# Performance work log

Measured on AMD Instinct MI355X. Metric: run time of the kernel, lower is better.

## Reference

```python
import jax, jax.numpy as jnp
import numpy as np

# config
HIDDEN = 1024
NUM_EXPERTS = 16
TOP_K = 4
MOE_INTER = 512
NUM_SHARED = 2
SHARED_INTER = MOE_INTER * NUM_SHARED  # 1024
NORM_TOPK = True
ROUTED_SCALE = 1.0
NUM_TOKENS = 1024


def setup_inputs() -> dict:
    key = jax.random.key(0)
    ks = jax.random.split(key, 8)
    s = 0.02
    return {
        "hidden_states": jax.random.normal(ks[0], (NUM_TOKENS, HIDDEN), jnp.float32),
        # router (BailingMoEGate): weight [E, H], no bias
        "router_w": jax.random.normal(ks[1], (NUM_EXPERTS, HIDDEN), jnp.float32) * s,
        # routed experts: gate/up proj [E, H, I], down proj [E, I, H]
        "w_gate": jax.random.normal(ks[2], (NUM_EXPERTS, HIDDEN, MOE_INTER), jnp.float32) * s,
        "w_up": jax.random.normal(ks[3], (NUM_EXPERTS, HIDDEN, MOE_INTER), jnp.float32) * s,
        "w_down": jax.random.normal(ks[4], (NUM_EXPERTS, MOE_INTER, HIDDEN), jnp.float32) * s,
        # shared experts (BailingMoEMLP, merged gate_up): [H, 2*Is], [Is, H]
        "ws_gate_up": jax.random.normal(ks[5], (HIDDEN, 2 * SHARED_INTER), jnp.float32) * s,
        "ws_down": jax.random.normal(ks[6], (SHARED_INTER, HIDDEN), jnp.float32) * s,
    }


def _moe_forward(x, router_w, w_gate, w_up, w_down, ws_gate_up, ws_down):
    T = x.shape[0]
    # ---- router: logits -> softmax -> top-k (score_function='softmax', no bias)
    logits = jnp.einsum("th,eh->te", x, router_w)          # [T, E]
    probs = jax.nn.softmax(logits, axis=-1)
    topk_w, topk_idx = jax.lax.top_k(probs, TOP_K)         # [T, K]
    if NORM_TOPK:
        topk_w = topk_w / jnp.sum(topk_w, axis=-1, keepdims=True)
    topk_w = topk_w * ROUTED_SCALE
    # sparse combine weights [T, E] (zeros for non-selected experts)
    combine = jnp.zeros((T, NUM_EXPERTS), x.dtype).at[
        jnp.arange(T)[:, None], topk_idx
    ].set(topk_w.astype(x.dtype))
    # ---- routed experts: SiLU(x W_gate) * (x W_up) then W_down, weighted combine
    g = jnp.einsum("th,ehi->tei", x, w_gate)               # [T, E, I]
    u = jnp.einsum("th,ehi->tei", x, w_up)
    h = jax.nn.silu(g) * u
    routed = jnp.einsum("tei,eih,te->th", h, w_down, combine)
    # ---- shared experts (dense SwiGLU MLP)
    gu = x @ ws_gate_up                                    # [T, 2*Is]
    g_s, u_s = jnp.split(gu, 2, axis=-1)
    shared = (jax.nn.silu(g_s) * u_s) @ ws_down
    return routed + shared


def reference(hidden_states, router_w, w_gate, w_up, w_down, ws_gate_up, ws_down):
    return _moe_forward(hidden_states, router_w, w_gate, w_up, w_down,
                        ws_gate_up, ws_down)
```

## Files before the change

kernel.cpp:

```cpp
#include <hip/hip_runtime.h>
#include <stdint.h>


typedef __attribute__((ext_vector_type(8))) unsigned short ushort8;
typedef __attribute__((ext_vector_type(4))) float f32x4;
typedef __attribute__((ext_vector_type(8))) __bf16 bf16x8;

#define T_TOK 1024
#define HID   1024
#define NEXP  16
#define TOPK  4
#define MINTER 512
#define SINTER 1024

constexpr size_t OFF_COUNTS = 0;
constexpr size_t OFF_LIST   = 1024;
constexpr size_t OFF_WT     = OFF_LIST  + 65536;
constexpr size_t OFF_TIDX   = OFF_WT    + 65536;
constexpr size_t OFF_XB     = OFF_TIDX  + 65536;
constexpr size_t OFF_HS     = OFF_XB    + 2097152;
constexpr size_t OFF_HR     = OFF_HS    + 2097152;
constexpr size_t OFF_WGT    = OFF_HR    + 4194304;
constexpr size_t OFF_WUT    = OFF_WGT   + 16777216;
constexpr size_t OFF_WDT    = OFF_WUT   + 16777216;
constexpr size_t OFF_WSGUT  = OFF_WDT   + 16777216;
constexpr size_t OFF_WSDT   = OFF_WSGUT + 4194304;
constexpr size_t OFF_ROUT   = OFF_WGT;

__device__ __forceinline__ unsigned short f2bf(float f) {
  union { float f; uint32_t u; } v; v.f = f;
  uint32_t r = (v.u + 0x7FFFu + ((v.u >> 16) & 1u)) >> 16;
  return (unsigned short)r;
}
__device__ __forceinline__ float bfu2f(uint32_t u) {
  union { uint32_t u; float f; } v; v.u = u << 16; return v.f;
}
__device__ __forceinline__ bf16x8 as_bf16x8(ushort8 s) {
  union { ushort8 s; bf16x8 b; } u; u.s = s; return u.b;
}
__device__ __forceinline__ float silu(float g) { return g / (1.f + __expf(-g)); }

__device__ __forceinline__ void glds16(const unsigned short* g, unsigned short* l) {
  __builtin_amdgcn_global_load_lds(
      (const __attribute__((address_space(1))) unsigned int*)g,
      (__attribute__((address_space(3))) unsigned int*)l, 16, 0, 0);
}

__global__ void init_kernel(int* counts) {
  if (threadIdx.x < NEXP) counts[threadIdx.x] = 0;
}

__global__ __launch_bounds__(64) void router_kernel(
    const float* __restrict__ x, const float* __restrict__ rw,
    int* counts, int* list, float* wt, int* tIdx,
    unsigned short* __restrict__ Xb) {
  const int t = blockIdx.x, l = threadIdx.x;
  float xv[16];
#pragma unroll
  for (int j = 0; j < 16; j++) xv[j] = x[t * HID + j * 64 + l];
#pragma unroll
  for (int j = 0; j < 16; j++) Xb[t * HID + j * 64 + l] = f2bf(xv[j]);
  float p[NEXP];
#pragma unroll
  for (int e = 0; e < NEXP; e++) {
    float s = 0.f;
#pragma unroll
    for (int j = 0; j < 16; j++) s += xv[j] * rw[e * HID + j * 64 + l];
#pragma unroll
    for (int off = 32; off > 0; off >>= 1) s += __shfl_xor(s, off);
    p[e] = s;
  }
  float mx = p[0];
#pragma unroll
  for (int e = 1; e < NEXP; e++) mx = fmaxf(mx, p[e]);
  int idx[TOPK]; float w4[TOPK]; float wsum = 0.f; unsigned used = 0u;
#pragma unroll
  for (int k = 0; k < TOPK; k++) {
    float bv = -1e30f; int bi = 0;
#pragma unroll
    for (int e = 0; e < NEXP; e++)
      if (!((used >> e) & 1u) && p[e] > bv) { bv = p[e]; bi = e; }
    used |= 1u << bi;
    idx[k] = bi;
    w4[k] = __expf(p[bi] - mx);
    wsum += w4[k];
  }
  const float inv = 1.f / wsum;
  if (l < TOPK) {
    const int e = idx[l];
    const int pos = atomicAdd(&counts[e], 1);
    list[e * 1024 + pos] = t;
    wt[e * 1024 + pos]   = w4[l] * inv;
    tIdx[t * TOPK + l]   = (e << 10) | pos;
  }
}

__global__ __launch_bounds__(256) void transpose_all_kernel(
    const float* __restrict__ Wg, const float* __restrict__ Wu,
    const float* __restrict__ Wd, const float* __restrict__ Wsgu,
    const float* __restrict__ Wsd,
    unsigned short* __restrict__ WgT, unsigned short* __restrict__ WuT,
    unsigned short* __restrict__ WdT, unsigned short* __restrict__ WsguT,
    unsigned short* __restrict__ WsdT) {
  const int bid = blockIdx.x;
  const float* src; unsigned short* dst; int R, C, tx, ty; size_t bo;
  if (bid < 4096) {
    const int which = bid >> 11, loc = bid & 2047;
    const int b = loc >> 7, t8 = loc & 127;
    src = which ? Wu : Wg; dst = which ? WuT : WgT;
    R = 1024; C = 512; bo = (size_t)b * R * C;
    tx = t8 & 7; ty = t8 >> 3;
  } else if (bid < 6144) {
    const int loc = bid - 4096, b = loc >> 7, t8 = loc & 127;
    src = Wd; dst = WdT; R = 512; C = 1024; bo = (size_t)b * R * C;
    tx = t8 & 15; ty = t8 >> 4;
  } else if (bid < 6656) {
    const int loc = bid - 6144;
    src = Wsgu; dst = WsguT; R = 1024; C = 2048; bo = 0;
    tx = loc & 31; ty = loc >> 5;
  } else {
    const int loc = bid - 6656;
    src = Wsd; dst = WsdT; R = 1024; C = 1024; bo = 0;
    tx = loc & 15; ty = loc >> 4;
  }
  __shared__ float tile[64][65];
  const int c0 = tx * 64, r0 = ty * 64, t = threadIdx.x;
  {
    const int r = t >> 4, c4 = (t & 15) * 4;
#pragma unroll
    for (int p = 0; p < 4; p++) {
      const int rr = p * 16 + r;
      const float4 v = *(const float4*)(src + bo + (size_t)(r0 + rr) * C + c0 + c4);
      tile[rr][c4 + 0] = v.x; tile[rr][c4 + 1] = v.y;
      tile[rr][c4 + 2] = v.z; tile[rr][c4 + 3] = v.w;
    }
  }
  __syncthreads();
  {
    const int c = t >> 2, rb = (t & 3) * 16;
#pragma unroll
    for (int s = 0; s < 4; s++) {
      const int rr = rb + 4 * s;
      union { unsigned short u[4]; uint2 v; } pk;
#pragma unroll
      for (int i = 0; i < 4; i++) pk.u[i] = f2bf(tile[rr + i][c]);
      *(uint2*)(dst + bo + (size_t)(c0 + c) * R + r0 + rr) = pk.v;
    }
  }
}

__global__ __launch_bounds__(256, 2) void phase1_kernel(
    const unsigned short* __restrict__ Xb,
    const unsigned short* __restrict__ WgT,
    const unsigned short* __restrict__ WuT,
    const unsigned short* __restrict__ WsguT,
    const int* __restrict__ counts, const int* __restrict__ list,
    const float* __restrict__ wt,
    unsigned short* __restrict__ Hr,
    unsigned short* __restrict__ Hs) {
  const int z = blockIdx.z, x = blockIdx.x, y = blockIdx.y;
  const bool routed = (z < NEXP);
  int cnt = 0, base = 0;
  if (routed) {
    if (x >= 4) return;
    cnt = counts[z];
    if (y * 128 >= cnt) return;
#pragma unroll
    for (int i = 0; i < NEXP; i++) base += (i < z) ? counts[i] : 0;
  }
  __shared__ __align__(16) unsigned short sA[2][128 * 32];
  __shared__ __align__(16) unsigned short sB[2][256 * 32];
  const int tid = threadIdx.x, w = tid >> 6, l = tid & 63;
  const int wm = w >> 1, wn = w & 1, m0 = y * 128;
  const int lg = ((l & 3) ^ ((l >> 3) & 3)) * 8;

  const unsigned short* aP[2];
#pragma unroll
  for (int ii = 0; ii < 2; ii++) {
    const int r = (2 * w + ii) * 16 + (l >> 2);
    const unsigned short* row;
    if (routed) row = Xb + (size_t)list[z * 1024 + min(m0 + r, cnt - 1)] * HID;
    else        row = Xb + (size_t)(m0 + r) * HID;
    aP[ii] = row + lg;
  }
  const unsigned short* bP[4];
#pragma unroll
  for (int ii = 0; ii < 4; ii++) {
    const int R = (4 * w + ii) * 16 + (l >> 2);
    const int col = x * 128 + (R & 127);
    const unsigned short* row;
    if (routed)
      row = ((R >= 128) ? WuT : WgT) + ((size_t)z * MINTER + col) * HID;
    else
      row = WsguT + ((size_t)((R >= 128) ? SINTER : 0) + col) * HID;
    bP[ii] = row + lg;
  }

  int aoff[4], boff[4];
#pragma unroll
  for (int i = 0; i < 4; i++) {
    const int m = wm * 64 + 16 * i + (l & 15);
    aoff[i] = m * 32 + (((l >> 4) ^ ((m >> 1) & 3)) * 8);
  }
#pragma unroll
  for (int j = 0; j < 4; j++) {
    const int n = wn * 64 + 16 * j + (l & 15);
    boff[j] = n * 32 + (((l >> 4) ^ ((n >> 1) & 3)) * 8);
  }

  f32x4 accG[4][4], accU[4][4];
#pragma unroll
  for (int i = 0; i < 4; i++)
#pragma unroll
    for (int j = 0; j < 4; j++) {
      accG[i][j] = (f32x4){0.f, 0.f, 0.f, 0.f};
      accU[i][j] = (f32x4){0.f, 0.f, 0.f, 0.f};
    }

  auto stage = [&](int k0, int bi) {
    unsigned short* A = sA[bi]; unsigned short* B = sB[bi];
#pragma unroll
    for (int ii = 0; ii < 2; ii++) glds16(aP[ii] + k0, A + (2 * w + ii) * 512);
#pragma unroll
    for (int ii = 0; ii < 4; ii++) glds16(bP[ii] + k0, B + (4 * w + ii) * 512);
  };

  stage(0, 0);
  const int steps = HID / 32;
  for (int s = 0; s < steps; s++) {
    __syncthreads();
    if (s + 1 < steps) stage((s + 1) * 32, (s + 1) & 1);
    const unsigned short* A = sA[s & 1];
    const unsigned short* B = sB[s & 1];
    bf16x8 af[4];
#pragma unroll
    for (int i = 0; i < 4; i++) af[i] = as_bf16x8(*(const ushort8*)(A + aoff[i]));
#pragma unroll
    for (int j = 0; j < 4; j++) {
      const bf16x8 gf = as_bf16x8(*(const ushort8*)(B + boff[j]));
      const bf16x8 uf = as_bf16x8(*(const ushort8*)(B + 128 * 32 + boff[j]));
#pragma unroll
      for (int i = 0; i < 4; i++) {
        accG[i][j] = __builtin_amdgcn_mfma_f32_16x16x32_bf16(af[i], gf, accG[i][j], 0, 0, 0);
        accU[i][j] = __builtin_amdgcn_mfma_f32_16x16x32_bf16(af[i], uf, accU[i][j], 0, 0, 0);
      }
    }
  }

#pragma unroll
  for (int i = 0; i < 4; i++)
#pragma unroll
    for (int r = 0; r < 4; r++) {
      const int row = wm * 64 + 16 * i + (l >> 4) * 4 + r;
      const int grow = m0 + row;
      if (routed) {
        if (grow < cnt) {
          const float wrow = wt[z * 1024 + grow];
#pragma unroll
          for (int j = 0; j < 4; j++) {
            const int col = x * 128 + wn * 64 + 16 * j + (l & 15);
            const float h = silu(accG[i][j][r]) * accU[i][j][r] * wrow;
            Hr[(size_t)(base + grow) * MINTER + col] = f2bf(h);
          }
        }
      } else {
#pragma unroll
        for (int j = 0; j < 4; j++) {
          const int col = x * 128 + wn * 64 + 16 * j + (l & 15);
          const float h = silu(accG[i][j][r]) * accU[i][j][r];
          Hs[(size_t)grow * SINTER + col] = f2bf(h);
        }
      }
    }
}

__global__ __launch_bounds__(256, 2) void phase2_kernel(
    const unsigned short* __restrict__ Hr, const unsigned short* __restrict__ Hs,
    const unsigned short* __restrict__ WdT,
    const unsigned short* __restrict__ WsdT,
    const int* __restrict__ counts,
    unsigned short* __restrict__ Rout,
    float* __restrict__ out) {
  const int z = blockIdx.z, x = blockIdx.x, y = blockIdx.y;
  const bool routed = (z < NEXP);
  int cnt = 0, base = 0, kdim;
  if (routed) {
    cnt = counts[z];
    if (y * 128 >= cnt) return;
#pragma unroll
    for (int i = 0; i < NEXP; i++) base += (i < z) ? counts[i] : 0;
    kdim = MINTER;
  } else {
    kdim = SINTER;
  }
  __shared__ __align__(16) unsigned short sA[2][128 * 32];
  __shared__ __align__(16) unsigned short sB[2][256 * 32];
  const int tid = threadIdx.x, w = tid >> 6, l = tid & 63;
  const int wm = w >> 1, wn = w & 1, m0 = y * 128;
  const int lg = ((l & 3) ^ ((l >> 3) & 3)) * 8;

  const unsigned short* aP[2];
#pragma unroll
  for (int ii = 0; ii < 2; ii++) {
    const int r = (2 * w + ii) * 16 + (l >> 2);
    const unsigned short* row;
    if (routed) row = Hr + (size_t)(base + min(m0 + r, cnt - 1)) * MINTER;
    else        row = Hs + (size_t)(m0 + r) * SINTER;
    aP[ii] = row + lg;
  }
  const unsigned short* bP[4];
#pragma unroll
  for (int ii = 0; ii < 4; ii++) {
    const int R = (4 * w + ii) * 16 + (l >> 2);
    const int col = x * 256 + R;
    const unsigned short* row =
        routed ? (WdT + ((size_t)z * HID + col) * MINTER)
               : (WsdT + (size_t)col * SINTER);
    bP[ii] = row + lg;
  }

  int aoff[4], boff[8];
#pragma unroll
  for (int i = 0; i < 4; i++) {
    const int m = wm * 64 + 16 * i + (l & 15);
    aoff[i] = m * 32 + (((l >> 4) ^ ((m >> 1) & 3)) * 8);
  }
#pragma unroll
  for (int j = 0; j < 8; j++) {
    const int n = wn * 128 + 16 * j + (l & 15);
    boff[j] = n * 32 + (((l >> 4) ^ ((n >> 1) & 3)) * 8);
  }

  f32x4 acc[4][8];
#pragma unroll
  for (int i = 0; i < 4; i++)
#pragma unroll
    for (int j = 0; j < 8; j++) acc[i][j] = (f32x4){0.f, 0.f, 0.f, 0.f};

  auto stage = [&](int k0, int bi) {
    unsigned short* A = sA[bi]; unsigned short* B = sB[bi];
#pragma unroll
    for (int ii = 0; ii < 2; ii++) glds16(aP[ii] + k0, A + (2 * w + ii) * 512);
#pragma unroll
    for (int ii = 0; ii < 4; ii++) glds16(bP[ii] + k0, B + (4 * w + ii) * 512);
  };

  stage(0, 0);
  const int steps = kdim / 32;
  for (int s = 0; s < steps; s++) {
    __syncthreads();
    if (s + 1 < steps) stage((s + 1) * 32, (s + 1) & 1);
    const unsigned short* A = sA[s & 1];
    const unsigned short* B = sB[s & 1];
    bf16x8 af[4];
#pragma unroll
    for (int i = 0; i < 4; i++) af[i] = as_bf16x8(*(const ushort8*)(A + aoff[i]));
#pragma unroll
    for (int j = 0; j < 8; j++) {
      const bf16x8 bfv = as_bf16x8(*(const ushort8*)(B + boff[j]));
#pragma unroll
      for (int i = 0; i < 4; i++)
        acc[i][j] = __builtin_amdgcn_mfma_f32_16x16x32_bf16(af[i], bfv, acc[i][j], 0, 0, 0);
    }
  }

#pragma unroll
  for (int i = 0; i < 4; i++)
#pragma unroll
    for (int r = 0; r < 4; r++) {
      const int row = wm * 64 + 16 * i + (l >> 4) * 4 + r;
      const int grow = m0 + row;
      if (routed) {
        if (grow < cnt) {
#pragma unroll
          for (int j = 0; j < 8; j++) {
            const int col = x * 256 + wn * 128 + 16 * j + (l & 15);
            Rout[(size_t)(base + grow) * HID + col] = f2bf(acc[i][j][r]);
          }
        }
      } else {
#pragma unroll
        for (int j = 0; j < 8; j++) {
          const int col = x * 256 + wn * 128 + 16 * j + (l & 15);
          out[(size_t)grow * HID + col] = acc[i][j][r];
        }
      }
    }
}

__global__ __launch_bounds__(256) void combine_kernel(
    const unsigned short* __restrict__ Rout, const int* __restrict__ counts,
    const int* __restrict__ tIdx, float* __restrict__ out) {
  __shared__ int sb[NEXP];
  if (threadIdx.x == 0) {
    int s = 0;
#pragma unroll
    for (int e = 0; e < NEXP; e++) { sb[e] = s; s += counts[e]; }
  }
  __syncthreads();
  const int t = blockIdx.x, c4 = threadIdx.x * 4;
  float4 o = *(const float4*)(out + (size_t)t * HID + c4);
#pragma unroll
  for (int k = 0; k < TOPK; k++) {
    const int v = tIdx[t * TOPK + k];
    const int row = sb[v >> 10] + (v & 1023);
    const uint2 rv = *(const uint2*)(Rout + (size_t)row * HID + c4);
    o.x += bfu2f(rv.x & 0xffffu); o.y += bfu2f(rv.x >> 16);
    o.z += bfu2f(rv.y & 0xffffu); o.w += bfu2f(rv.y >> 16);
  }
  *(float4*)(out + (size_t)t * HID + c4) = o;
}

extern "C" void kernel_launch(void* const* d_in, const int* in_sizes, int n_in,
                              void* d_out, int out_size, void* d_ws, size_t ws_size,
                              hipStream_t stream) {
  const float* x      = (const float*)d_in[0];
  const float* rw     = (const float*)d_in[1];
  const float* w_gate = (const float*)d_in[2];
  const float* w_up   = (const float*)d_in[3];
  const float* w_down = (const float*)d_in[4];
  const float* ws_gu  = (const float*)d_in[5];
  const float* ws_dn  = (const float*)d_in[6];
  float* out = (float*)d_out;
  char* ws = (char*)d_ws;

  int*   counts = (int*)  (ws + OFF_COUNTS);
  int*   list   = (int*)  (ws + OFF_LIST);
  float* wtbuf  = (float*)(ws + OFF_WT);
  int*   tIdx   = (int*)  (ws + OFF_TIDX);
  unsigned short* Xb    = (unsigned short*)(ws + OFF_XB);
  unsigned short* Hs    = (unsigned short*)(ws + OFF_HS);
  unsigned short* Hr    = (unsigned short*)(ws + OFF_HR);
  unsigned short* WgT   = (unsigned short*)(ws + OFF_WGT);
  unsigned short* WuT   = (unsigned short*)(ws + OFF_WUT);
  unsigned short* WdT   = (unsigned short*)(ws + OFF_WDT);
  unsigned short* WsguT = (unsigned short*)(ws + OFF_WSGUT);
  unsigned short* WsdT  = (unsigned short*)(ws + OFF_WSDT);
  unsigned short* Rout  = (unsigned short*)(ws + OFF_ROUT);

  init_kernel<<<1, 64, 0, stream>>>(counts);
  router_kernel<<<T_TOK, 64, 0, stream>>>(x, rw, counts, list, wtbuf, tIdx, Xb);
  transpose_all_kernel<<<6912, 256, 0, stream>>>(
      w_gate, w_up, w_down, ws_gu, ws_dn, WgT, WuT, WdT, WsguT, WsdT);
  phase1_kernel<<<dim3(8, 8, 17), 256, 0, stream>>>(
      Xb, WgT, WuT, WsguT, counts, list, wtbuf, Hr, Hs);
  phase2_kernel<<<dim3(4, 8, 17), 256, 0, stream>>>(
      Hr, Hs, WdT, WsdT, counts, Rout, out);
  combine_kernel<<<T_TOK, 256, 0, stream>>>(Rout, counts, tIdx, out);
  (void)in_sizes; (void)n_in; (void)out_size; (void)ws_size;
}
```

Measured before the change: 296.3 us.

## Replace LDS-staged GEMM tiles with direct global-to-register triple-buffered loads

Both expert GEMM kernels stop staging A and B tiles through shared memory with global_load_lds and barriers. Each wave now loads its MFMA fragments straight from global memory into registers, keeping a three-deep register pipeline, and launch bounds drop to one block per SIMD slot to free registers. This removes LDS traffic and __syncthreads, but tiles are no longer shared across waves, so each wave re-reads data from global memory or cache. The loads are strided 16-byte per lane rather than coalesced, and occupancy is lower.

```diff
diff --git a/kernel.cpp b/kernel.cpp
--- a/kernel.cpp
+++ b/kernel.cpp
@@ -39,12 +39,6 @@
   union { ushort8 s; bf16x8 b; } u; u.s = s; return u.b;
 }
 __device__ __forceinline__ float silu(float g) { return g / (1.f + __expf(-g)); }
-
-__device__ __forceinline__ void glds16(const unsigned short* g, unsigned short* l) {
-  __builtin_amdgcn_global_load_lds(
-      (const __attribute__((address_space(1))) unsigned int*)g,
-      (__attribute__((address_space(3))) unsigned int*)l, 16, 0, 0);
-}
 
 __global__ void init_kernel(int* counts) {
   if (threadIdx.x < NEXP) counts[threadIdx.x] = 0;
@@ -149,7 +143,7 @@
   }
 }
 
-__global__ __launch_bounds__(256, 2) void phase1_kernel(
+__global__ __launch_bounds__(256, 1) void phase1_kernel(
     const unsigned short* __restrict__ Xb,
     const unsigned short* __restrict__ WgT,
     const unsigned short* __restrict__ WuT,
@@ -168,44 +162,28 @@
 #pragma unroll
     for (int i = 0; i < NEXP; i++) base += (i < z) ? counts[i] : 0;
   }
-  __shared__ __align__(16) unsigned short sA[2][128 * 32];
-  __shared__ __align__(16) unsigned short sB[2][256 * 32];
   const int tid = threadIdx.x, w = tid >> 6, l = tid & 63;
   const int wm = w >> 1, wn = w & 1, m0 = y * 128;
-  const int lg = ((l & 3) ^ ((l >> 3) & 3)) * 8;
-
-  const unsigned short* aP[2];
-#pragma unroll
-  for (int ii = 0; ii < 2; ii++) {
-    const int r = (2 * w + ii) * 16 + (l >> 2);
-    const unsigned short* row;
-    if (routed) row = Xb + (size_t)list[z * 1024 + min(m0 + r, cnt - 1)] * HID;
-    else        row = Xb + (size_t)(m0 + r) * HID;
-    aP[ii] = row + lg;
-  }
-  const unsigned short* bP[4];
-#pragma unroll
-  for (int ii = 0; ii < 4; ii++) {
-    const int R = (4 * w + ii) * 16 + (l >> 2);
-    const int col = x * 128 + (R & 127);
-    const unsigned short* row;
-    if (routed)
-      row = ((R >= 128) ? WuT : WgT) + ((size_t)z * MINTER + col) * HID;
-    else
-      row = WsguT + ((size_t)((R >= 128) ? SINTER : 0) + col) * HID;
-    bP[ii] = row + lg;
-  }
-
-  int aoff[4], boff[4];
+  const int kq = (l >> 4) * 8;
+
+  const unsigned short* aP[4];
 #pragma unroll
   for (int i = 0; i < 4; i++) {
-    const int m = wm * 64 + 16 * i + (l & 15);
-    aoff[i] = m * 32 + (((l >> 4) ^ ((m >> 1) & 3)) * 8);
-  }
+    const int row = m0 + wm * 64 + 16 * i + (l & 15);
+    if (routed) aP[i] = Xb + (size_t)list[z * 1024 + min(row, cnt - 1)] * HID + kq;
+    else        aP[i] = Xb + (size_t)row * HID + kq;
+  }
+  const unsigned short *gP[4], *uP[4];
 #pragma unroll
   for (int j = 0; j < 4; j++) {
-    const int n = wn * 64 + 16 * j + (l & 15);
-    boff[j] = n * 32 + (((l >> 4) ^ ((n >> 1) & 3)) * 8);
+    const int n = x * 128 + wn * 64 + 16 * j + (l & 15);
+    if (routed) {
+      gP[j] = WgT + ((size_t)z * MINTER + n) * HID + kq;
+      uP[j] = WuT + ((size_t)z * MINTER + n) * HID + kq;
+    } else {
+      gP[j] = WsguT + (size_t)n * HID + kq;
+      uP[j] = WsguT + (size_t)(SINTER + n) * HID + kq;
+    }
   }
 
   f32x4 accG[4][4], accU[4][4];
@@ -217,35 +195,35 @@
       accU[i][j] = (f32x4){0.f, 0.f, 0.f, 0.f};
     }
 
-  auto stage = [&](int k0, int bi) {
-    unsigned short* A = sA[bi]; unsigned short* B = sB[bi];
-#pragma unroll
-    for (int ii = 0; ii < 2; ii++) glds16(aP[ii] + k0, A + (2 * w + ii) * 512);
-#pragma unroll
-    for (int ii = 0; ii < 4; ii++) glds16(bP[ii] + k0, B + (4 * w + ii) * 512);
-  };
-
-  stage(0, 0);
+  ushort8 Af[3][4], Gf[3][4], Uf[3][4];
+#define P1_LD(st, k0)                                                   \
+  {                                                                     \
+    _Pragma("unroll") for (int i = 0; i < 4; i++)                       \
+        Af[st][i] = *(const ushort8*)(aP[i] + (k0));                    \
+    _Pragma("unroll") for (int j = 0; j < 4; j++) {                     \
+      Gf[st][j] = *(const ushort8*)(gP[j] + (k0));                      \
+      Uf[st][j] = *(const ushort8*)(uP[j] + (k0));                      \
+    }                                                                   \
+  }
+  P1_LD(0, 0) P1_LD(1, 32) P1_LD(2, 64)
   const int steps = HID / 32;
+#pragma unroll 1
   for (int s = 0; s < steps; s++) {
-    __syncthreads();
-    if (s + 1 < steps) stage((s + 1) * 32, (s + 1) & 1);
-    const unsigned short* A = sA[s & 1];
-    const unsigned short* B = sB[s & 1];
-    bf16x8 af[4];
-#pragma unroll
-    for (int i = 0; i < 4; i++) af[i] = as_bf16x8(*(const ushort8*)(A + aoff[i]));
+    const int cur = s % 3;
 #pragma unroll
     for (int j = 0; j < 4; j++) {
-      const bf16x8 gf = as_bf16x8(*(const ushort8*)(B + boff[j]));
-      const bf16x8 uf = as_bf16x8(*(const ushort8*)(B + 128 * 32 + boff[j]));
+      const bf16x8 gf = as_bf16x8(Gf[cur][j]);
+      const bf16x8 uf = as_bf16x8(Uf[cur][j]);
 #pragma unroll
       for (int i = 0; i < 4; i++) {
-        accG[i][j] = __builtin_amdgcn_mfma_f32_16x16x32_bf16(af[i], gf, accG[i][j], 0, 0, 0);
-        accU[i][j] = __builtin_amdgcn_mfma_f32_16x16x32_bf16(af[i], uf, accU[i][j], 0, 0, 0);
+        const bf16x8 af = as_bf16x8(Af[cur][i]);
+        accG[i][j] = __builtin_amdgcn_mfma_f32_16x16x32_bf16(af, gf, accG[i][j], 0, 0, 0);
+        accU[i][j] = __builtin_amdgcn_mfma_f32_16x16x32_bf16(af, uf, accU[i][j], 0, 0, 0);
       }
     }
-  }
+    if (s + 3 < steps) P1_LD(cur, (s + 3) * 32)
+  }
+#undef P1_LD
 
 #pragma unroll
   for (int i = 0; i < 4; i++)
@@ -274,7 +252,7 @@
     }
 }
 
-__global__ __launch_bounds__(256, 2) void phase2_kernel(
+__global__ __launch_bounds__(256, 1) void phase2_kernel(
     const unsigned short* __restrict__ Hr, const unsigned short* __restrict__ Hs,
     const unsigned short* __restrict__ WdT,
     const unsigned short* __restrict__ WsdT,
@@ -293,42 +271,23 @@
   } else {
     kdim = SINTER;
   }
-  __shared__ __align__(16) unsigned short sA[2][128 * 32];
-  __shared__ __align__(16) unsigned short sB[2][256 * 32];
   const int tid = threadIdx.x, w = tid >> 6, l = tid & 63;
   const int wm = w >> 1, wn = w & 1, m0 = y * 128;
-  const int lg = ((l & 3) ^ ((l >> 3) & 3)) * 8;
-
-  const unsigned short* aP[2];
-#pragma unroll
-  for (int ii = 0; ii < 2; ii++) {
-    const int r = (2 * w + ii) * 16 + (l >> 2);
-    const unsigned short* row;
-    if (routed) row = Hr + (size_t)(base + min(m0 + r, cnt - 1)) * MINTER;
-    else        row = Hs + (size_t)(m0 + r) * SINTER;
-    aP[ii] = row + lg;
-  }
-  const unsigned short* bP[4];
-#pragma unroll
-  for (int ii = 0; ii < 4; ii++) {
-    const int R = (4 * w + ii) * 16 + (l >> 2);
-    const int col = x * 256 + R;
-    const unsigned short* row =
-        routed ? (WdT + ((size_t)z * HID + col) * MINTER)
-               : (WsdT + (size_t)col * SINTER);
-    bP[ii] = row + lg;
-  }
-
-  int aoff[4], boff[8];
+  const int kq = (l >> 4) * 8;
+
+  const unsigned short* aP[4];
 #pragma unroll
   for (int i = 0; i < 4; i++) {
-    const int m = wm * 64 + 16 * i + (l & 15);
-    aoff[i] = m * 32 + (((l >> 4) ^ ((m >> 1) & 3)) * 8);
-  }
+    const int row = m0 + wm * 64 + 16 * i + (l & 15);
+    if (routed) aP[i] = Hr + (size_t)(base + min(row, cnt - 1)) * MINTER + kq;
+    else        aP[i] = Hs + (size_t)row * SINTER + kq;
+  }
+  const unsigned short* bP[8];
 #pragma unroll
   for (int j = 0; j < 8; j++) {
-    const int n = wn * 128 + 16 * j + (l & 15);
-    boff[j] = n * 32 + (((l >> 4) ^ ((n >> 1) & 3)) * 8);
+    const int n = x * 256 + wn * 128 + 16 * j + (l & 15);
+    bP[j] = routed ? (WdT + ((size_t)z * HID + n) * MINTER + kq)
+                   : (WsdT + (size_t)n * SINTER + kq);
   }
 
   f32x4 acc[4][8];
@@ -337,32 +296,31 @@
 #pragma unroll
     for (int j = 0; j < 8; j++) acc[i][j] = (f32x4){0.f, 0.f, 0.f, 0.f};
 
-  auto stage = [&](int k0, int bi) {
-    unsigned short* A = sA[bi]; unsigned short* B = sB[bi];
-#pragma unroll
-    for (int ii = 0; ii < 2; ii++) glds16(aP[ii] + k0, A + (2 * w + ii) * 512);
-#pragma unroll
-    for (int ii = 0; ii < 4; ii++) glds16(bP[ii] + k0, B + (4 * w + ii) * 512);
-  };
-
-  stage(0, 0);
+  ushort8 Af[3][4], Bf[3][8];
+#define P2_LD(st, k0)                                                   \
+  {                                                                     \
+    _Pragma("unroll") for (int i = 0; i < 4; i++)                       \
+        Af[st][i] = *(const ushort8*)(aP[i] + (k0));                    \
+    _Pragma("unroll") for (int j = 0; j < 8; j++)                       \
+        Bf[st][j] = *(const ushort8*)(bP[j] + (k0));                    \
+  }
+  P2_LD(0, 0) P2_LD(1, 32) P2_LD(2, 64)
   const int steps = kdim / 32;
+#pragma unroll 1
   for (int s = 0; s < steps; s++) {
-    __syncthreads();
-    if (s + 1 < steps) stage((s + 1) * 32, (s + 1) & 1);
-    const unsigned short* A = sA[s & 1];
-    const unsigned short* B = sB[s & 1];
-    bf16x8 af[4];
-#pragma unroll
-    for (int i = 0; i < 4; i++) af[i] = as_bf16x8(*(const ushort8*)(A + aoff[i]));
+    const int cur = s % 3;
 #pragma unroll
     for (int j = 0; j < 8; j++) {
-      const bf16x8 bfv = as_bf16x8(*(const ushort8*)(B + boff[j]));
-#pragma unroll
-      for (int i = 0; i < 4; i++)
-        acc[i][j] = __builtin_amdgcn_mfma_f32_16x16x32_bf16(af[i], bfv, acc[i][j], 0, 0, 0);
-    }
-  }
+      const bf16x8 bfv = as_bf16x8(Bf[cur][j]);
+#pragma unroll
+      for (int i = 0; i < 4; i++) {
+        const bf16x8 af = as_bf16x8(Af[cur][i]);
+        acc[i][j] = __builtin_amdgcn_mfma_f32_16x16x32_bf16(af, bfv, acc[i][j], 0, 0, 0);
+      }
+    }
+    if (s + 3 < steps) P2_LD(cur, (s + 3) * 32)
+  }
+#undef P2_LD
 
 #pragma unroll
   for (int i = 0; i < 4; i++)
```

After: 770.0 us. 2.6x slower.

## Triple-buffer GEMM LDS pipeline with explicit vmcnt waits and drop swizzle

Applied to the files above, without the earlier changes.

Both grouped GEMM kernels move from a double-buffered LDS pipeline with __syncthreads to a three-stage ring. Loads are issued two steps ahead and gated with an explicit s_waitcnt vmcnt(12) plus barrier, so more global-to-LDS traffic stays in flight. The XOR swizzle on LDS offsets is removed, which can raise bank conflicts, and the weight-transpose kernel now writes 16-byte packed stores instead of 8-byte ones. The larger LDS footprint (about 72KB per block) may limit the two-blocks-per-CU occupancy target, and the wrapped prefetch at the tail issues redundant loads.

```diff
diff --git a/kernel.cpp b/kernel.cpp
--- a/kernel.cpp
+++ b/kernel.cpp
@@ -45,6 +45,9 @@
       (const __attribute__((address_space(1))) unsigned int*)g,
       (__attribute__((address_space(3))) unsigned int*)l, 16, 0, 0);
 }
+
+#define PIPE_WAIT() asm volatile("s_waitcnt vmcnt(12)\ns_barrier" ::: "memory")
+#define PIPE_SYNC() asm volatile("s_waitcnt lgkmcnt(0)\ns_barrier" ::: "memory")
 
 __global__ void init_kernel(int* counts) {
   if (threadIdx.x < NEXP) counts[threadIdx.x] = 0;
@@ -136,16 +139,13 @@
     }
   }
   __syncthreads();
-  {
-    const int c = t >> 2, rb = (t & 3) * 16;
-#pragma unroll
-    for (int s = 0; s < 4; s++) {
-      const int rr = rb + 4 * s;
-      union { unsigned short u[4]; uint2 v; } pk;
-#pragma unroll
-      for (int i = 0; i < 4; i++) pk.u[i] = f2bf(tile[rr + i][c]);
-      *(uint2*)(dst + bo + (size_t)(c0 + c) * R + r0 + rr) = pk.v;
-    }
+#pragma unroll
+  for (int half = 0; half < 2; half++) {
+    const int c = half * 32 + (t >> 3), r8 = (t & 7) * 8;
+    union { unsigned short u[8]; ushort8 v; } pk;
+#pragma unroll
+    for (int i = 0; i < 8; i++) pk.u[i] = f2bf(tile[r8 + i][c]);
+    *(ushort8*)(dst + bo + (size_t)(c0 + c) * R + r0 + r8) = pk.v;
   }
 }
 
@@ -168,45 +168,36 @@
 #pragma unroll
     for (int i = 0; i < NEXP; i++) base += (i < z) ? counts[i] : 0;
   }
-  __shared__ __align__(16) unsigned short sA[2][128 * 32];
-  __shared__ __align__(16) unsigned short sB[2][256 * 32];
+  __shared__ __align__(16) unsigned short sA[3][128 * 32];
+  __shared__ __align__(16) unsigned short sB[3][256 * 32];
   const int tid = threadIdx.x, w = tid >> 6, l = tid & 63;
   const int wm = w >> 1, wn = w & 1, m0 = y * 128;
-  const int lg = ((l & 3) ^ ((l >> 3) & 3)) * 8;
-
-  const unsigned short* aP[2];
+
+  const unsigned short* aS[2];
 #pragma unroll
   for (int ii = 0; ii < 2; ii++) {
-    const int r = (2 * w + ii) * 16 + (l >> 2);
+    const int r = 32 * w + 16 * ii + (l >> 2);
     const unsigned short* row;
     if (routed) row = Xb + (size_t)list[z * 1024 + min(m0 + r, cnt - 1)] * HID;
     else        row = Xb + (size_t)(m0 + r) * HID;
-    aP[ii] = row + lg;
-  }
-  const unsigned short* bP[4];
+    aS[ii] = row + (l & 3) * 8;
+  }
+  const unsigned short* bS[4];
 #pragma unroll
   for (int ii = 0; ii < 4; ii++) {
-    const int R = (4 * w + ii) * 16 + (l >> 2);
+    const int R = 64 * w + 16 * ii + (l >> 2);
     const int col = x * 128 + (R & 127);
     const unsigned short* row;
-    if (routed)
-      row = ((R >= 128) ? WuT : WgT) + ((size_t)z * MINTER + col) * HID;
-    else
-      row = WsguT + ((size_t)((R >= 128) ? SINTER : 0) + col) * HID;
-    bP[ii] = row + lg;
-  }
-
-  int aoff[4], boff[4];
-#pragma unroll
-  for (int i = 0; i < 4; i++) {
-    const int m = wm * 64 + 16 * i + (l & 15);
-    aoff[i] = m * 32 + (((l >> 4) ^ ((m >> 1) & 3)) * 8);
-  }
-#pragma unroll
-  for (int j = 0; j < 4; j++) {
-    const int n = wn * 64 + 16 * j + (l & 15);
-    boff[j] = n * 32 + (((l >> 4) ^ ((n >> 1) & 3)) * 8);
-  }
+    if (routed) row = ((R >= 128) ? WuT : WgT) + ((size_t)z * MINTER + col) * HID;
+    else        row = WsguT + (size_t)(((R >= 128) ? SINTER : 0) + col) * HID;
+    bS[ii] = row + (l & 3) * 8;
+  }
+
+  int aOff[4], bOff[4];
+#pragma unroll
+  for (int i = 0; i < 4; i++) aOff[i] = (wm * 64 + 16 * i + (l & 15)) * 32 + (l >> 4) * 8;
+#pragma unroll
+  for (int j = 0; j < 4; j++) bOff[j] = (wn * 64 + 16 * j + (l & 15)) * 32 + (l >> 4) * 8;
 
   f32x4 accG[4][4], accU[4][4];
 #pragma unroll
@@ -217,34 +208,36 @@
       accU[i][j] = (f32x4){0.f, 0.f, 0.f, 0.f};
     }
 
-  auto stage = [&](int k0, int bi) {
-    unsigned short* A = sA[bi]; unsigned short* B = sB[bi];
-#pragma unroll
-    for (int ii = 0; ii < 2; ii++) glds16(aP[ii] + k0, A + (2 * w + ii) * 512);
-#pragma unroll
-    for (int ii = 0; ii < 4; ii++) glds16(bP[ii] + k0, B + (4 * w + ii) * 512);
+  auto stage = [&](int k0, int b) {
+#pragma unroll
+    for (int ii = 0; ii < 2; ii++) glds16(aS[ii] + k0, &sA[b][(32 * w + 16 * ii) * 32]);
+#pragma unroll
+    for (int ii = 0; ii < 4; ii++) glds16(bS[ii] + k0, &sB[b][(64 * w + 16 * ii) * 32]);
   };
 
-  stage(0, 0);
+  stage(0, 0); stage(32, 1); stage(64, 2);
   const int steps = HID / 32;
+#pragma unroll 1
   for (int s = 0; s < steps; s++) {
-    __syncthreads();
-    if (s + 1 < steps) stage((s + 1) * 32, (s + 1) & 1);
-    const unsigned short* A = sA[s & 1];
-    const unsigned short* B = sB[s & 1];
+    PIPE_WAIT();
+    const int cb = s % 3;
+    const unsigned short* A = &sA[cb][0];
+    const unsigned short* B = &sB[cb][0];
     bf16x8 af[4];
 #pragma unroll
-    for (int i = 0; i < 4; i++) af[i] = as_bf16x8(*(const ushort8*)(A + aoff[i]));
+    for (int i = 0; i < 4; i++) af[i] = as_bf16x8(*(const ushort8*)(A + aOff[i]));
 #pragma unroll
     for (int j = 0; j < 4; j++) {
-      const bf16x8 gf = as_bf16x8(*(const ushort8*)(B + boff[j]));
-      const bf16x8 uf = as_bf16x8(*(const ushort8*)(B + 128 * 32 + boff[j]));
+      const bf16x8 gf = as_bf16x8(*(const ushort8*)(B + bOff[j]));
+      const bf16x8 uf = as_bf16x8(*(const ushort8*)(B + 128 * 32 + bOff[j]));
 #pragma unroll
       for (int i = 0; i < 4; i++) {
         accG[i][j] = __builtin_amdgcn_mfma_f32_16x16x32_bf16(af[i], gf, accG[i][j], 0, 0, 0);
         accU[i][j] = __builtin_amdgcn_mfma_f32_16x16x32_bf16(af[i], uf, accU[i][j], 0, 0, 0);
       }
     }
+    PIPE_SYNC();
+    stage(((s + 3) & (steps - 1)) * 32, cb);
   }
 
 #pragma unroll
@@ -293,43 +286,36 @@
   } else {
     kdim = SINTER;
   }
-  __shared__ __align__(16) unsigned short sA[2][128 * 32];
-  __shared__ __align__(16) unsigned short sB[2][256 * 32];
+  __shared__ __align__(16) unsigned short sA[3][128 * 32];
+  __shared__ __align__(16) unsigned short sB[3][256 * 32];
   const int tid = threadIdx.x, w = tid >> 6, l = tid & 63;
   const int wm = w >> 1, wn = w & 1, m0 = y * 128;
-  const int lg = ((l & 3) ^ ((l >> 3) & 3)) * 8;
-
-  const unsigned short* aP[2];
+
+  const unsigned short* aS[2];
 #pragma unroll
   for (int ii = 0; ii < 2; ii++) {
-    const int r = (2 * w + ii) * 16 + (l >> 2);
+    const int r = 32 * w + 16 * ii + (l >> 2);
     const unsigned short* row;
     if (routed) row = Hr + (size_t)(base + min(m0 + r, cnt - 1)) * MINTER;
     else        row = Hs + (size_t)(m0 + r) * SINTER;
-    aP[ii] = row + lg;
-  }
-  const unsigned short* bP[4];
+    aS[ii] = row + (l & 3) * 8;
+  }
+  const unsigned short* bS[4];
 #pragma unroll
   for (int ii = 0; ii < 4; ii++) {
-    const int R = (4 * w + ii) * 16 + (l >> 2);
+    const int R = 64 * w + 16 * ii + (l >> 2);
     const int col = x * 256 + R;
     const unsigned short* row =
         routed ? (WdT + ((size_t)z * HID + col) * MINTER)
                : (WsdT + (size_t)col * SINTER);
-    bP[ii] = row + lg;
-  }
-
-  int aoff[4], boff[8];
-#pragma unroll
-  for (int i = 0; i < 4; i++) {
-    const int m = wm * 64 + 16 * i + (l & 15);
-    aoff[i] = m * 32 + (((l >> 4) ^ ((m >> 1) & 3)) * 8);
-  }
-#pragma unroll
-  for (int j = 0; j < 8; j++) {
-    const int n = wn * 128 + 16 * j + (l & 15);
-    boff[j] = n * 32 + (((l >> 4) ^ ((n >> 1) & 3)) * 8);
-  }
+    bS[ii] = row + (l & 3) * 8;
+  }
+
+  int aOff[4], bOff[8];
+#pragma unroll
+  for (int i = 0; i < 4; i++) aOff[i] = (wm * 64 + 16 * i + (l & 15)) * 32 + (l >> 4) * 8;
+#pragma unroll
+  for (int j = 0; j < 8; j++) bOff[j] = (wn * 128 + 16 * j + (l & 15)) * 32 + (l >> 4) * 8;
 
   f32x4 acc[4][8];
 #pragma unroll
@@ -337,31 +323,33 @@
 #pragma unroll
     for (int j = 0; j < 8; j++) acc[i][j] = (f32x4){0.f, 0.f, 0.f, 0.f};
 
-  auto stage = [&](int k0, int bi) {
-    unsigned short* A = sA[bi]; unsigned short* B = sB[bi];
-#pragma unroll
-    for (int ii = 0; ii < 2; ii++) glds16(aP[ii] + k0, A + (2 * w + ii) * 512);
-#pragma unroll
-    for (int ii = 0; ii < 4; ii++) glds16(bP[ii] + k0, B + (4 * w + ii) * 512);
+  auto stage = [&](int k0, int b) {
+#pragma unroll
+    for (int ii = 0; ii < 2; ii++) glds16(aS[ii] + k0, &sA[b][(32 * w + 16 * ii) * 32]);
+#pragma unroll
+    for (int ii = 0; ii < 4; ii++) glds16(bS[ii] + k0, &sB[b][(64 * w + 16 * ii) * 32]);
   };
 
-  stage(0, 0);
+  stage(0, 0); stage(32, 1); stage(64, 2);
   const int steps = kdim / 32;
+#pragma unroll 1
   for (int s = 0; s < steps; s++) {
-    __syncthreads();
-    if (s + 1 < steps) stage((s + 1) * 32, (s + 1) & 1);
-    const unsigned short* A = sA[s & 1];
-    const unsigned short* B = sB[s & 1];
+    PIPE_WAIT();
+    const int cb = s % 3;
+    const unsigned short* A = &sA[cb][0];
+    const unsigned short* B = &sB[cb][0];
     bf16x8 af[4];
 #pragma unroll
-    for (int i = 0; i < 4; i++) af[i] = as_bf16x8(*(const ushort8*)(A + aoff[i]));
+    for (int i = 0; i < 4; i++) af[i] = as_bf16x8(*(const ushort8*)(A + aOff[i]));
 #pragma unroll
     for (int j = 0; j < 8; j++) {
-      const bf16x8 bfv = as_bf16x8(*(const ushort8*)(B + boff[j]));
+      const bf16x8 bfv = as_bf16x8(*(const ushort8*)(B + bOff[j]));
 #pragma unroll
       for (int i = 0; i < 4; i++)
         acc[i][j] = __builtin_amdgcn_mfma_f32_16x16x32_bf16(af[i], bfv, acc[i][j], 0, 0, 0);
     }
+    PIPE_SYNC();
+    stage(((s + 3) & (steps - 1)) * 32, cb);
   }
 
 #pragma unroll
```

New measurement: 281.4 us. 1.05x faster.
